# Kernel optimization log

Measured on AMD Instinct MI355X. Metric: run time of the kernel, lower is better.

## Reference

```python
import jax, jax.numpy as jnp
import numpy as np

N_NODES = 40000
N_EDGES = 640000
N_GRAPHS = 64
F_IN = 32       # fourier_order*4
D_EMB = 256     # int(0.5*512)
D_HID = 512     # int(0.5*1024)
D_FC = 1024     # int(0.5*2048)
N_CLS = 10


def setup_inputs() -> dict:
    key = jax.random.key(0)
    ks = iter(jax.random.split(key, 40))
    rn = lambda shape, s=0.05: jax.random.normal(next(ks), shape, jnp.float32) * s
    inp = {
        'x': jax.random.normal(next(ks), (N_NODES, F_IN), jnp.float32),
        'edge_index': jax.random.randint(next(ks), (2, N_EDGES), 0, N_NODES, jnp.int32),
        'edge_attr': jax.random.uniform(next(ks), (N_EDGES, 1), jnp.float32),
        'batch': jnp.sort(jax.random.randint(next(ks), (N_NODES,), 0, N_GRAPHS, jnp.int32)),
        # embedding MLP
        'emb_w1': rn((F_IN, D_EMB)), 'emb_b1': jnp.zeros((D_EMB,), jnp.float32),
        'emb_w2': rn((D_EMB, D_EMB)), 'emb_b2': jnp.zeros((D_EMB,), jnp.float32),
        # edge_proj MLP
        'ep_w1': rn((1, 64)), 'ep_b1': jnp.zeros((64,), jnp.float32),
        'ep_w2': rn((64, 1)), 'ep_b2': jnp.zeros((1,), jnp.float32),
        # GCNConv weights (x @ W + b, PyG convention)
        'w_c1': rn((D_EMB, D_HID)), 'b_c1': jnp.zeros((D_HID,), jnp.float32),
        'w_c2': rn((D_HID, D_HID)), 'b_c2': jnp.zeros((D_HID,), jnp.float32),
        'w_c3': rn((D_HID, D_HID)), 'b_c3': jnp.zeros((D_HID,), jnp.float32),
        'w_c4': rn((D_HID, D_HID)), 'b_c4': jnp.zeros((D_HID,), jnp.float32),
        'w_c5': rn((D_HID, D_HID)), 'b_c5': jnp.zeros((D_HID,), jnp.float32),
        'w_c6': rn((D_HID, D_HID)), 'b_c6': jnp.zeros((D_HID,), jnp.float32),
        # head
        'fc1_w': rn((D_HID, D_FC)), 'fc1_b': jnp.zeros((D_FC,), jnp.float32),
        'head_w': rn((D_FC, N_CLS)), 'head_b': jnp.zeros((N_CLS,), jnp.float32),
    }
    return inp


def _gcn_conv(x, src, dst, norm, W, b):
    # PyG GCNConv: linear transform, then normalized scatter-add aggregation, then bias
    h = x @ W                                   # [N, d_out]
    msg = h[src] * norm[:, None]                # [E+N, d_out] gathered messages
    agg = jax.ops.segment_sum(msg, dst, num_segments=N_NODES)
    return agg + b


def _forward(x, edge_attr, emb_w1, emb_b1, emb_w2, emb_b2, ep_w1, ep_b1, ep_w2, ep_b2,
             w_c1, b_c1, w_c2, b_c2, w_c3, b_c3, w_c4, b_c4, w_c5, b_c5, w_c6, b_c6,
             fc1_w, fc1_b, head_w, head_b, edge_index, batch):
    # edge weights from edge_proj MLP (sigmoid output in (0,1))
    ew = jax.nn.sigmoid(jax.nn.relu(edge_attr @ ep_w1 + ep_b1) @ ep_w2 + ep_b2)[:, 0]  # [E]
    # gcn_norm with self loops (identical for every conv layer -> compute once)
    loops = jnp.arange(N_NODES, dtype=edge_index.dtype)
    src = jnp.concatenate([edge_index[0], loops])
    dst = jnp.concatenate([edge_index[1], loops])
    w = jnp.concatenate([ew, jnp.ones((N_NODES,), ew.dtype)])
    deg = jax.ops.segment_sum(w, dst, num_segments=N_NODES)
    dinv = jnp.where(deg > 0, jax.lax.rsqrt(jnp.maximum(deg, 1e-12)), 0.0)
    norm = dinv[src] * w * dinv[dst]            # [E+N]

    h = jax.nn.relu(jax.nn.relu(x @ emb_w1 + emb_b1) @ emb_w2 + emb_b2)
    h = _gcn_conv(h, src, dst, norm, w_c1, b_c1)
    skip = jax.nn.relu(h)
    h = _gcn_conv(skip, src, dst, norm, w_c2, b_c2)
    h = jax.nn.relu(h)
    h = _gcn_conv(h, src, dst, norm, w_c3, b_c3)
    skip = jax.nn.relu(h) + skip                # has_skip=True
    h = _gcn_conv(skip, src, dst, norm, w_c4, b_c4)  # is_deep=True
    h = jax.nn.relu(h)
    h = _gcn_conv(h, src, dst, norm, w_c5, b_c5)
    h = jax.nn.relu(h)
    h = _gcn_conv(h, src, dst, norm, w_c6, b_c6)
    skip = jax.nn.relu(h) + skip

    # global mean pool over graphs
    sums = jax.ops.segment_sum(skip, batch, num_segments=N_GRAPHS)
    cnts = jax.ops.segment_sum(jnp.ones((N_NODES,), skip.dtype), batch, num_segments=N_GRAPHS)
    pooled = sums / jnp.maximum(cnts, 1.0)[:, None]   # [G, D_HID]

    out = jax.nn.relu(pooled @ fc1_w + fc1_b) @ head_w + head_b   # [G, N_CLS]
    return out


def reference(x, edge_index, edge_attr, batch, emb_w1, emb_b1, emb_w2, emb_b2,
              ep_w1, ep_b1, ep_w2, ep_b2, w_c1, b_c1, w_c2, b_c2, w_c3, b_c3,
              w_c4, b_c4, w_c5, b_c5, w_c6, b_c6, fc1_w, fc1_b, head_w, head_b):
    return _forward(x, edge_attr, emb_w1, emb_b1, emb_w2, emb_b2, ep_w1, ep_b1, ep_w2, ep_b2,
                    w_c1, b_c1, w_c2, b_c2, w_c3, b_c3, w_c4, b_c4, w_c5, b_c5, w_c6, b_c6,
                    fc1_w, fc1_b, head_w, head_b, edge_index, batch)
```

## Files before the change

### kernel.cpp

```cpp
#include <hip/hip_runtime.h>
#include <math.h>

#define N_NODES 40000
#define MP      40192
#define NROWB   157
#define N_EDGES 640000
#define N_GRAPHS 64
#define F_IN 32
#define D_EMB 256
#define D_HID 512
#define D_FC 1024
#define N_CLS 10

typedef _Float16 f16x8 __attribute__((ext_vector_type(8)));
typedef float f32x4  __attribute__((ext_vector_type(4)));
typedef unsigned short u16;

template <int N> struct VecU;
template <> struct VecU<2> { typedef unsigned T __attribute__((ext_vector_type(2))); };
template <> struct VecU<4> { typedef unsigned T __attribute__((ext_vector_type(4))); };

__device__ __forceinline__ float h2f(u16 u) {
    union { u16 s; _Float16 h; } v; v.s = u; return (float)v.h;
}
__device__ __forceinline__ u16 f2h(float f) {
    union { u16 s; _Float16 h; } v; v.h = (_Float16)f; return v.s;
}
__device__ __forceinline__ void async16(void* lds, const void* g) {
    __builtin_amdgcn_global_load_lds((const __attribute__((address_space(1))) void*)g,
                                     (__attribute__((address_space(3))) void*)lds, 16, 0, 0);
}

__device__ __forceinline__ int pk_idx(int r, int q) {
    int rp = r >> 1;
    int g  = (((r & 1) << 2) | q) ^ (rp & 7);
    return rp * 64 + g * 8;
}

__global__ void prep_all(const float* __restrict__ x, u16* __restrict__ xb, u16* __restrict__ G,
                         float* __restrict__ deg, int* __restrict__ cnt, int* __restrict__ cursor,
                         float* __restrict__ sums) {
    int i = blockIdx.x * blockDim.x + threadIdx.x;
    if (i < N_NODES) { deg[i] = 1.0f; cnt[i] = 0; cursor[i] = 0; }
    if (i < MP * F_IN) {
        int row = i >> 5, colk = i & 31;
        float v = (row < N_NODES) ? x[i] : 0.f;
        size_t idx = (size_t)(row >> 8) * 8192 + pk_idx(row & 255, colk >> 3) + (colk & 7);
        xb[idx] = f2h(v);
    }
    if (i < 16 * 3072) {
        int kc = i / 3072, rem = i % 3072;
        G[(size_t)(156 * 16 + kc) * 8192 + 5120 + rem] = 0;
    } else if (i < 16 * 3072 + 8 * 3072) {
        int j = i - 16 * 3072;
        int kc = j / 3072, rem = j % 3072;
        G[(size_t)(156 * 8 + kc) * 8192 + 5120 + rem] = 0;
    }
    if (i < N_GRAPHS * D_HID) sums[i] = 0.f;
}

__global__ void edge_mlp_deg(const float* __restrict__ edge_attr,
                             const float* __restrict__ ep_w1, const float* __restrict__ ep_b1,
                             const float* __restrict__ ep_w2, const float* __restrict__ ep_b2,
                             const int* __restrict__ dst,
                             float* __restrict__ ew, float* __restrict__ deg, int* __restrict__ cnt) {
    __shared__ float w1[64], b1[64], w2[64];
    int t = threadIdx.x;
    if (t < 64) { w1[t] = ep_w1[t]; b1[t] = ep_b1[t]; w2[t] = ep_w2[t]; }
    __syncthreads();
    int e = blockIdx.x * blockDim.x + t;
    if (e >= N_EDGES) return;
    float x = edge_attr[e];
    float s = ep_b2[0];
#pragma unroll
    for (int j = 0; j < 64; ++j) s += fmaxf(x * w1[j] + b1[j], 0.f) * w2[j];
    float sig = 1.f / (1.f + expf(-s));
    ew[e] = sig;
    int d = dst[e];
    atomicAdd(&deg[d], sig);
    atomicAdd(&cnt[d], 1);
}

__global__ void dinv_kernel(const float* __restrict__ deg, float* __restrict__ dinv,
                            float* __restrict__ nloop) {
    int i = blockIdx.x * blockDim.x + threadIdx.x;
    if (i >= N_NODES) return;
    float d = deg[i];
    float r = (d > 0.f) ? rsqrtf(fmaxf(d, 1e-12f)) : 0.f;
    dinv[i] = r;
    nloop[i] = r * r;
}

__global__ void scan_kernel(const int* __restrict__ cnt, int* __restrict__ rowptr) {
    __shared__ int part[1024];
    int t = threadIdx.x;
    const int PER = (N_NODES + 1023) / 1024;
    int base = t * PER;
    int s = 0;
    for (int k = 0; k < PER; ++k) { int i = base + k; if (i < N_NODES) s += cnt[i]; }
    part[t] = s;
    __syncthreads();
    for (int off = 1; off < 1024; off <<= 1) {
        int v = (t >= off) ? part[t - off] : 0;
        __syncthreads();
        part[t] += v;
        __syncthreads();
    }
    int run = (t == 0) ? 0 : part[t - 1];
    for (int k = 0; k < PER; ++k) {
        int i = base + k;
        if (i < N_NODES) { rowptr[i] = run; run += cnt[i]; }
    }
    if (t == 1023) rowptr[N_NODES] = run;
}

__global__ void fill_csr_kernel(const int* __restrict__ src, const int* __restrict__ dst,
                                const float* __restrict__ ew, const float* __restrict__ dinv,
                                const int* __restrict__ rowptr, int* __restrict__ cursor,
                                int2* __restrict__ cv) {
    int e = blockIdx.x * blockDim.x + threadIdx.x;
    if (e >= N_EDGES) return;
    int d = dst[e];
    int s = src[e];
    float n = dinv[s] * ew[e] * dinv[d];
    int p = rowptr[d] + atomicAdd(&cursor[d], 1);
    cv[p] = make_int2(s, __float_as_int(n));
}

struct WPair { const float* s; u16* d; int K; int N; };
struct WP8 { WPair m[8]; };

__global__ void wprep_all(WP8 a) {
    __shared__ u16 th[32][33];
    WPair w = a.m[blockIdx.z];
    int n0 = blockIdx.x * 32;
    int k0 = blockIdx.y * 32;
    if (n0 >= w.N || k0 >= w.K) return;
    int tx = threadIdx.x, ty = threadIdx.y;
#pragma unroll
    for (int r = 0; r < 4; ++r) {
        int k = ty + r * 8;
        th[k][tx] = f2h(w.s[(size_t)(k0 + k) * w.N + n0 + tx]);
    }
    __syncthreads();
#pragma unroll
    for (int r = 0; r < 4; ++r) {
        int n = ty + r * 8;
        int R = n0 + n;
        int kcol = k0 + tx;
        size_t idx = ((size_t)(R >> 7) * (w.K >> 5) + (kcol >> 5)) * 4096
                   + pk_idx(R & 127, (kcol >> 3) & 3) + (kcol & 7);
        w.d[idx] = th[tx][n];
    }
}

__launch_bounds__(512)
__global__ void mfma_gemm(const u16* __restrict__ A,
                          const u16* __restrict__ W,
                          const float* __restrict__ bias,
                          const u16* __restrict__ skip,
                          u16* __restrict__ C, u16* __restrict__ Cpk,
                          int K, int N,
                          const int* __restrict__ batch, float* __restrict__ pool) {
    __shared__ __align__(16) u16 smem[2 * 12288];
    __shared__ int sbatch[128];

    int nColB = N >> 7;
    int b = blockIdx.x;
    int rowI = (b >> 3) / nColB * 8 + (b & 7);
    int colI = (b >> 3) % nColB;
    if (rowI >= NROWB) return;
    int rowBase = rowI * 256;
    int colBase = colI * 128;

    int t = threadIdx.x;
    int lane = t & 63;
    int wave = t >> 6;
    int wr = wave >> 1;
    int wc = wave & 1;

    int quad = lane >> 4;
    int mrow = lane & 15;

    const u16* pA = A + (size_t)rowI * (K >> 5) * 8192 + wave * 1024 + (lane << 3);
    const u16* pW = W + (size_t)colI * (K >> 5) * 4096 + wave * 512 + (lane << 3);

    f32x4 acc[4][4] = {};

    int nIter = K >> 5;
    {
        u16* As = smem; u16* Ws = smem + 8192;
        async16(&As[wave * 1024], pA);
        async16(&As[wave * 1024 + 512], pA + 512);
        async16(&Ws[wave * 512], pW);
    }

    for (int it = 0; it < nIter; ++it) {
        int cur = it & 1;
        __builtin_amdgcn_s_barrier();
        if (it + 1 < nIter) {
            u16* As = smem + (cur ^ 1) * 12288; u16* Ws = As + 8192;
            const u16* sA = pA + (size_t)(it + 1) * 8192;
            const u16* sW = pW + (size_t)(it + 1) * 4096;
            async16(&As[wave * 1024], sA);
            async16(&As[wave * 1024 + 512], sA + 512);
            async16(&Ws[wave * 512], sW);
            asm volatile("s_waitcnt vmcnt(3)" ::: "memory");
        } else {
            asm volatile("s_waitcnt vmcnt(0)" ::: "memory");
        }
        __builtin_amdgcn_sched_barrier(0);
        __builtin_amdgcn_s_barrier();
        __builtin_amdgcn_sched_barrier(0);

        const u16* As = smem + cur * 12288;
        const u16* Ws = As + 8192;
        f16x8 af[4], wf[4];
#pragma unroll
        for (int i = 0; i < 4; ++i) {
            int Ra = wr * 64 + i * 16 + mrow;
            int sa = ((Ra & 1) * 4 + quad) ^ ((Ra >> 1) & 7);
            af[i] = *(const f16x8*)&As[(Ra >> 1) * 64 + sa * 8];
            int Rb = wc * 64 + i * 16 + mrow;
            int sb = ((Rb & 1) * 4 + quad) ^ ((Rb >> 1) & 7);
            wf[i] = *(const f16x8*)&Ws[(Rb >> 1) * 64 + sb * 8];
        }
#pragma unroll
        for (int i = 0; i < 4; ++i)
#pragma unroll
            for (int j = 0; j < 4; ++j)
                acc[i][j] = __builtin_amdgcn_mfma_f32_16x16x32_f16(af[i], wf[j], acc[i][j], 0, 0, 0);
    }
    __syncthreads();

    const int ES = 132;
    u16* eb = smem;
#pragma unroll
    for (int ph = 0; ph < 2; ++ph) {
        if ((wr >> 1) == ph) {
#pragma unroll
            for (int j = 0; j < 4; ++j) {
                int col = colBase + wc * 64 + j * 16 + mrow;
                float bv = bias[col];
#pragma unroll
                for (int i = 0; i < 4; ++i) {
#pragma unroll
                    for (int r = 0; r < 4; ++r) {
                        int lr = (wr & 1) * 64 + i * 16 + quad * 4 + r;
                        size_t row = (size_t)rowBase + ph * 128 + lr;
                        float v = fmaxf(acc[i][j][r] + bv, 0.f);
                        if (skip) v += h2f(skip[row * N + col]);
                        eb[lr * ES + wc * 64 + j * 16 + mrow] = f2h(v);
                    }
                }
            }
        }
        if (pool && t < 128) {
            int row = rowBase + ph * 128 + t;
            sbatch[t] = (row < N_NODES) ? batch[row] : -1;
        }
        __syncthreads();
        if (C) {
#pragma unroll
            for (int k2 = 0; k2 < 4; ++k2) {
                int c = t + k2 * 512;
                int row = c >> 4;
                int ch = c & 15;
                f16x8 v = *(const f16x8*)&eb[row * ES + ch * 8];
                *(f16x8*)&C[(size_t)(rowBase + ph * 128 + row) * N + colBase + ch * 8] = v;
            }
        } else if (Cpk) {
#pragma unroll
            for (int k2 = 0; k2 < 4; ++k2) {
                int c = t + k2 * 512;
                int row = c >> 4;
                int ch = c & 15;
                f16x8 v = *(const f16x8*)&eb[row * ES + ch * 8];
                size_t idx = ((size_t)rowI * (N >> 5) + (colBase >> 5) + (ch >> 2)) * 8192
                           + pk_idx(ph * 128 + row, ch & 3);
                *(f16x8*)&Cpk[idx] = v;
            }
        }
        if (pool) {
            int c = t & 127;
            int rs = (t >> 7) * 32;
            float run = 0.f; int g = -1;
            for (int r = rs; r < rs + 32; ++r) {
                int bg = sbatch[r];
                if (bg != g) {
                    if (g >= 0) atomicAdd(&pool[(size_t)g * D_HID + colBase + c], run);
                    run = 0.f; g = bg;
                }
                if (bg >= 0) run += h2f(eb[r * ES + c]);
            }
            if (g >= 0) atomicAdd(&pool[(size_t)g * D_HID + colBase + c], run);
        }
        __syncthreads();
    }
}

template <int D>
__launch_bounds__(256)
__global__ void gather_f16(const u16* __restrict__ h, const int* __restrict__ rowptr,
                           const int2* __restrict__ cv, const float* __restrict__ nloop,
                           u16* __restrict__ out) {
    constexpr int FPL = D / 64;
    constexpr int UPL = FPL / 2;
    using VU = typename VecU<UPL>::T;
    int node = blockIdx.x * 4 + (threadIdx.x >> 6);
    int lane = threadIdx.x & 63;
    if (node >= N_NODES) return;
    union UU { unsigned u; _Float16 h[2]; };
    float acc[FPL];
    float sl = nloop[node];
    {
        VU own = *(const VU*)(h + (size_t)node * D + lane * FPL);
#pragma unroll
        for (int u = 0; u < UPL; ++u) {
            UU w; w.u = own[u];
            acc[2 * u]     = (float)w.h[0] * sl;
            acc[2 * u + 1] = (float)w.h[1] * sl;
        }
    }
    int beg = rowptr[node], end = rowptr[node + 1];
    if (end > beg) {
        int last = end - 1;
        int2 c[8];
#pragma unroll
        for (int m = 0; m < 8; ++m) c[m] = cv[min(beg + m, last)];
        for (int j = beg; j < end; j += 8) {
            VU tv[8];
#pragma unroll
            for (int m = 0; m < 8; ++m)
                tv[m] = *(const VU*)(h + (size_t)c[m].x * D + lane * FPL);
            int jn = j + 8;
            int2 cn[8];
#pragma unroll
            for (int m = 0; m < 8; ++m) cn[m] = c[m];
            if (jn < end) {
#pragma unroll
                for (int m = 0; m < 8; ++m) cn[m] = cv[min(jn + m, last)];
            }
            __builtin_amdgcn_sched_barrier(0);
#pragma unroll
            for (int m = 0; m < 8; ++m) {
                float v = (j + m < end) ? __int_as_float(c[m].y) : 0.f;
#pragma unroll
                for (int u = 0; u < UPL; ++u) {
                    UU w; w.u = tv[m][u];
                    acc[2 * u]     += (float)w.h[0] * v;
                    acc[2 * u + 1] += (float)w.h[1] * v;
                }
            }
#pragma unroll
            for (int m = 0; m < 8; ++m) c[m] = cn[m];
        }
    }
    VU o;
#pragma unroll
    for (int u = 0; u < UPL; ++u) {
        unsigned lo = f2h(acc[2 * u]);
        unsigned hi = f2h(acc[2 * u + 1]);
        o[u] = lo | (hi << 16);
    }
    size_t blkb = (size_t)(node >> 8) * (D >> 5);
    int rr = node & 255;
    if (D == 512) {
        size_t idx = (blkb + (lane >> 2)) * 8192 + pk_idx(rr, lane & 3);
        *(VU*)(out + idx) = o;
    } else {
        size_t idx = (blkb + (lane >> 3)) * 8192 + pk_idx(rr, (lane >> 1) & 3) + (lane & 1) * 4;
        *(VU*)(out + idx) = o;
    }
}

__launch_bounds__(1024)
__global__ void fc1_head(const float* __restrict__ sums, const int* __restrict__ batch,
                         const float* __restrict__ fc1_w, const float* __restrict__ fc1_b,
                         const float* __restrict__ head_w, const float* __restrict__ head_b,
                         float* __restrict__ out) {
    __shared__ float sv[D_HID];
    __shared__ float hacc[N_CLS];
    __shared__ float invc;
    int g = blockIdx.x;
    int t = threadIdx.x;
    if (t == 0) {
        int lo = 0, hi = N_NODES;
        while (lo < hi) { int m = (lo + hi) >> 1; if (batch[m] < g) lo = m + 1; else hi = m; }
        int lb = lo;
        lo = lb; hi = N_NODES;
        while (lo < hi) { int m = (lo + hi) >> 1; if (batch[m] < g + 1) lo = m + 1; else hi = m; }
        invc = 1.f / fmaxf((float)(lo - lb), 1.f);
    }
    if (t < N_CLS) hacc[t] = 0.f;
    __syncthreads();
    if (t < D_HID) sv[t] = sums[(size_t)g * D_HID + t] * invc;
    __syncthreads();
    int j = t;
    float acc = fc1_b[j];
#pragma unroll 8
    for (int k = 0; k < D_HID; ++k) acc += sv[k] * fc1_w[(size_t)k * D_FC + j];
    float f = fmaxf(acc, 0.f);
    float p[N_CLS];
#pragma unroll
    for (int c = 0; c < N_CLS; ++c) p[c] = f * head_w[j * N_CLS + c];
#pragma unroll
    for (int c = 0; c < N_CLS; ++c) {
        float v = p[c];
        for (int off = 32; off; off >>= 1) v += __shfl_down(v, off, 64);
        if ((t & 63) == 0) atomicAdd(&hacc[c], v);
    }
    __syncthreads();
    if (t < N_CLS) out[g * N_CLS + t] = hacc[t] + head_b[t];
}

extern "C" void kernel_launch(void* const* d_in, const int* in_sizes, int n_in,
                              void* d_out, int out_size, void* d_ws, size_t ws_size,
                              hipStream_t stream) {
    const float* x          = (const float*)d_in[0];
    const int*   edge_index = (const int*)d_in[1];
    const float* edge_attr  = (const float*)d_in[2];
    const int*   batch      = (const int*)d_in[3];
    const float* emb_w1 = (const float*)d_in[4];
    const float* emb_b1 = (const float*)d_in[5];
    const float* emb_w2 = (const float*)d_in[6];
    const float* emb_b2 = (const float*)d_in[7];
    const float* ep_w1  = (const float*)d_in[8];
    const float* ep_b1  = (const float*)d_in[9];
    const float* ep_w2  = (const float*)d_in[10];
    const float* ep_b2  = (const float*)d_in[11];
    const float* w_c[6] = { (const float*)d_in[12], (const float*)d_in[14], (const float*)d_in[16],
                            (const float*)d_in[18], (const float*)d_in[20], (const float*)d_in[22] };
    const float* b_c[6] = { (const float*)d_in[13], (const float*)d_in[15], (const float*)d_in[17],
                            (const float*)d_in[19], (const float*)d_in[21], (const float*)d_in[23] };
    const float* fc1_w  = (const float*)d_in[24];
    const float* fc1_b  = (const float*)d_in[25];
    const float* head_w = (const float*)d_in[26];
    const float* head_b = (const float*)d_in[27];
    float* out = (float*)d_out;

    const int* src = edge_index;
    const int* dst = edge_index + N_EDGES;

    char* p = (char*)d_ws;
    auto alloc = [&](size_t bytes) { char* r = p; p += (bytes + 255) & ~(size_t)255; return r; };
    float* ew    = (float*)alloc(N_EDGES * 4);
    float* deg   = (float*)alloc(N_NODES * 4);
    float* dinv  = (float*)alloc(N_NODES * 4);
    float* nloop = (float*)alloc(N_NODES * 4);
    int* cnt     = (int*)alloc(N_NODES * 4);
    int* cursor  = (int*)alloc(N_NODES * 4);
    int* rowptr  = (int*)alloc((N_NODES + 1) * 4);
    int2* cv     = (int2*)alloc((size_t)N_EDGES * 8);
    u16* xb = (u16*)alloc((size_t)MP * F_IN * 2);
    u16* H1 = (u16*)alloc((size_t)MP * D_EMB * 2);
    u16* H2 = (u16*)alloc((size_t)MP * D_EMB * 2);
    u16* G  = (u16*)alloc((size_t)MP * D_HID * 2);
    u16* S1 = (u16*)alloc((size_t)MP * D_HID * 2);
    u16* S2 = (u16*)alloc((size_t)MP * D_HID * 2);
    u16* Cb = (u16*)alloc((size_t)MP * D_HID * 2);
    u16* we1 = (u16*)alloc((size_t)F_IN * D_EMB * 2);
    u16* we2 = (u16*)alloc((size_t)D_EMB * D_EMB * 2);
    u16* wc[6];
    wc[0] = (u16*)alloc((size_t)D_EMB * D_HID * 2);
    for (int i = 1; i < 6; ++i) wc[i] = (u16*)alloc((size_t)D_HID * D_HID * 2);
    float* sums = (float*)alloc(N_GRAPHS * D_HID * 4);

    const int TB = 256;
    const int EB = (N_EDGES + TB - 1) / TB;
    const int NB = (N_NODES + TB - 1) / TB;

    prep_all<<<(MP * F_IN + TB - 1) / TB, TB, 0, stream>>>(x, xb, G, deg, cnt, cursor, sums);
    edge_mlp_deg<<<EB, TB, 0, stream>>>(edge_attr, ep_w1, ep_b1, ep_w2, ep_b2, dst, ew, deg, cnt);
    dinv_kernel<<<NB, TB, 0, stream>>>(deg, dinv, nloop);
    scan_kernel<<<1, 1024, 0, stream>>>(cnt, rowptr);
    fill_csr_kernel<<<EB, TB, 0, stream>>>(src, dst, ew, dinv, rowptr, cursor, cv);

    WP8 wp;
    wp.m[0] = { emb_w1, we1, F_IN,  D_EMB };
    wp.m[1] = { emb_w2, we2, D_EMB, D_EMB };
    wp.m[2] = { w_c[0], wc[0], D_EMB, D_HID };
    for (int i = 1; i < 6; ++i) wp.m[2 + i] = { w_c[i], wc[i], D_HID, D_HID };
    wprep_all<<<dim3(16, 16, 8), dim3(32, 8), 0, stream>>>(wp);

    const int SLOTS = ((NROWB + 7) / 8) * 8;
    const int GRID2 = SLOTS * (D_EMB / 128);
    const int GRID4 = SLOTS * (D_HID / 128);
    mfma_gemm<<<GRID2, 512, 0, stream>>>(xb, we1, emb_b1, nullptr, nullptr, H1, F_IN, D_EMB, nullptr, nullptr);
    mfma_gemm<<<GRID2, 512, 0, stream>>>(H1, we2, emb_b2, nullptr, H2, nullptr, D_EMB, D_EMB, nullptr, nullptr);

    const int GG = (N_NODES + 3) / 4;
    gather_f16<D_EMB><<<GG, 256, 0, stream>>>(H2, rowptr, cv, nloop, G);
    mfma_gemm<<<GRID4, 512, 0, stream>>>(G, wc[0], b_c[0], nullptr, S1, nullptr, D_EMB, D_HID, nullptr, nullptr);
    gather_f16<D_HID><<<GG, 256, 0, stream>>>(S1, rowptr, cv, nloop, G);
    mfma_gemm<<<GRID4, 512, 0, stream>>>(G, wc[1], b_c[1], nullptr, Cb, nullptr, D_HID, D_HID, nullptr, nullptr);
    gather_f16<D_HID><<<GG, 256, 0, stream>>>(Cb, rowptr, cv, nloop, G);
    mfma_gemm<<<GRID4, 512, 0, stream>>>(G, wc[2], b_c[2], S1, S2, nullptr, D_HID, D_HID, nullptr, nullptr);
    gather_f16<D_HID><<<GG, 256, 0, stream>>>(S2, rowptr, cv, nloop, G);
    mfma_gemm<<<GRID4, 512, 0, stream>>>(G, wc[3], b_c[3], nullptr, Cb, nullptr, D_HID, D_HID, nullptr, nullptr);
    gather_f16<D_HID><<<GG, 256, 0, stream>>>(Cb, rowptr, cv, nloop, G);
    mfma_gemm<<<GRID4, 512, 0, stream>>>(G, wc[4], b_c[4], nullptr, Cb, nullptr, D_HID, D_HID, nullptr, nullptr);
    gather_f16<D_HID><<<GG, 256, 0, stream>>>(Cb, rowptr, cv, nloop, G);
    mfma_gemm<<<GRID4, 512, 0, stream>>>(G, wc[5], b_c[5], S2, nullptr, nullptr, D_HID, D_HID, batch, sums);

    fc1_head<<<N_GRAPHS, 1024, 0, stream>>>(sums, batch, fc1_w, fc1_b, head_w, head_b, out);
}
```

Before: 1.206 ms.

## Restructure GEMM to narrow 32-column tiles with full-K weight slice in LDS

The MFMA GEMM switches from 256x128 tiles, where both A and W are double-buffered through LDS, to 256x32 tiles. The whole K-extent weight slice is preloaded into LDS once, and each wave streams its A fragments straight from global memory into registers with software prefetch. This removes per-iteration barriers and LDS staging of A, and the grid grows fourfold for more parallelism. In exchange, each A row block is re-read from global memory by four times as many blocks and per-block MFMA reuse drops, so the kernel may become bandwidth-bound.

```diff
diff --git a/kernel.cpp b/kernel.cpp
--- a/kernel.cpp
+++ b/kernel.cpp
@@ -162,95 +162,99 @@
                           u16* __restrict__ C, u16* __restrict__ Cpk,
                           int K, int N,
                           const int* __restrict__ batch, float* __restrict__ pool) {
-    __shared__ __align__(16) u16 smem[2 * 12288];
+    __shared__ __align__(16) u16 Wl[16384];
     __shared__ int sbatch[128];
 
-    int nColB = N >> 7;
+    const int nColB = N >> 5;
     int b = blockIdx.x;
     int rowI = (b >> 3) / nColB * 8 + (b & 7);
     int colI = (b >> 3) % nColB;
     if (rowI >= NROWB) return;
     int rowBase = rowI * 256;
-    int colBase = colI * 128;
+    int colBase = colI * 32;
 
     int t = threadIdx.x;
     int lane = t & 63;
     int wave = t >> 6;
-    int wr = wave >> 1;
-    int wc = wave & 1;
-
     int quad = lane >> 4;
     int mrow = lane & 15;
-
-    const u16* pA = A + (size_t)rowI * (K >> 5) * 8192 + wave * 1024 + (lane << 3);
-    const u16* pW = W + (size_t)colI * (K >> 5) * 4096 + wave * 512 + (lane << 3);
-
-    f32x4 acc[4][4] = {};
-
     int nIter = K >> 5;
+
+    int sw = (((mrow & 1) << 2) | quad) ^ ((mrow >> 1) & 7);
+    int laneA = (wave * 16 + (mrow >> 1)) * 64 + sw * 8;
+    int laneW = (mrow >> 1) * 64 + sw * 8;
+
+    const u16* pA = A + (size_t)rowI * nIter * 8192;
+
+    f16x8 aA0 = *(const f16x8*)&pA[laneA];
+    f16x8 aA1 = *(const f16x8*)&pA[laneA + 512];
+    f16x8 aB0, aB1;
+
     {
-        u16* As = smem; u16* Ws = smem + 8192;
-        async16(&As[wave * 1024], pA);
-        async16(&As[wave * 1024 + 512], pA + 512);
-        async16(&Ws[wave * 512], pW);
-    }
-
-    for (int it = 0; it < nIter; ++it) {
-        int cur = it & 1;
-        __builtin_amdgcn_s_barrier();
+        const u16* ws = W + ((size_t)(colI >> 2) * nIter) * 4096 + (colI & 3) * 1024;
+        for (int kc = wave; kc < nIter; kc += 8) {
+            const u16* s = ws + (size_t)kc * 4096;
+            async16(&Wl[kc * 1024],       s + lane * 8);
+            async16(&Wl[kc * 1024 + 512], s + 512 + lane * 8);
+        }
+    }
+    asm volatile("s_waitcnt vmcnt(0)" ::: "memory");
+    __syncthreads();
+
+    f32x4 acc[2][2] = {};
+
+    for (int it = 0; it < nIter; it += 2) {
         if (it + 1 < nIter) {
-            u16* As = smem + (cur ^ 1) * 12288; u16* Ws = As + 8192;
-            const u16* sA = pA + (size_t)(it + 1) * 8192;
-            const u16* sW = pW + (size_t)(it + 1) * 4096;
-            async16(&As[wave * 1024], sA);
-            async16(&As[wave * 1024 + 512], sA + 512);
-            async16(&Ws[wave * 512], sW);
-            asm volatile("s_waitcnt vmcnt(3)" ::: "memory");
-        } else {
-            asm volatile("s_waitcnt vmcnt(0)" ::: "memory");
+            const u16* nA = pA + (size_t)(it + 1) * 8192;
+            aB0 = *(const f16x8*)&nA[laneA];
+            aB1 = *(const f16x8*)&nA[laneA + 512];
         }
         __builtin_amdgcn_sched_barrier(0);
-        __builtin_amdgcn_s_barrier();
-        __builtin_amdgcn_sched_barrier(0);
-
-        const u16* As = smem + cur * 12288;
-        const u16* Ws = As + 8192;
-        f16x8 af[4], wf[4];
-#pragma unroll
-        for (int i = 0; i < 4; ++i) {
-            int Ra = wr * 64 + i * 16 + mrow;
-            int sa = ((Ra & 1) * 4 + quad) ^ ((Ra >> 1) & 7);
-            af[i] = *(const f16x8*)&As[(Ra >> 1) * 64 + sa * 8];
-            int Rb = wc * 64 + i * 16 + mrow;
-            int sb = ((Rb & 1) * 4 + quad) ^ ((Rb >> 1) & 7);
-            wf[i] = *(const f16x8*)&Ws[(Rb >> 1) * 64 + sb * 8];
-        }
-#pragma unroll
-        for (int i = 0; i < 4; ++i)
-#pragma unroll
-            for (int j = 0; j < 4; ++j)
-                acc[i][j] = __builtin_amdgcn_mfma_f32_16x16x32_f16(af[i], wf[j], acc[i][j], 0, 0, 0);
-    }
-    __syncthreads();
-
-    const int ES = 132;
-    u16* eb = smem;
+        {
+            const u16* Wc = &Wl[it * 1024];
+            f16x8 w0 = *(const f16x8*)&Wc[laneW];
+            f16x8 w1 = *(const f16x8*)&Wc[laneW + 512];
+            acc[0][0] = __builtin_amdgcn_mfma_f32_16x16x32_f16(aA0, w0, acc[0][0], 0, 0, 0);
+            acc[0][1] = __builtin_amdgcn_mfma_f32_16x16x32_f16(aA0, w1, acc[0][1], 0, 0, 0);
+            acc[1][0] = __builtin_amdgcn_mfma_f32_16x16x32_f16(aA1, w0, acc[1][0], 0, 0, 0);
+            acc[1][1] = __builtin_amdgcn_mfma_f32_16x16x32_f16(aA1, w1, acc[1][1], 0, 0, 0);
+        }
+        if (it + 1 < nIter) {
+            if (it + 2 < nIter) {
+                const u16* nA = pA + (size_t)(it + 2) * 8192;
+                aA0 = *(const f16x8*)&nA[laneA];
+                aA1 = *(const f16x8*)&nA[laneA + 512];
+            }
+            __builtin_amdgcn_sched_barrier(0);
+            const u16* Wc = &Wl[(it + 1) * 1024];
+            f16x8 w0 = *(const f16x8*)&Wc[laneW];
+            f16x8 w1 = *(const f16x8*)&Wc[laneW + 512];
+            acc[0][0] = __builtin_amdgcn_mfma_f32_16x16x32_f16(aB0, w0, acc[0][0], 0, 0, 0);
+            acc[0][1] = __builtin_amdgcn_mfma_f32_16x16x32_f16(aB0, w1, acc[0][1], 0, 0, 0);
+            acc[1][0] = __builtin_amdgcn_mfma_f32_16x16x32_f16(aB1, w0, acc[1][0], 0, 0, 0);
+            acc[1][1] = __builtin_amdgcn_mfma_f32_16x16x32_f16(aB1, w1, acc[1][1], 0, 0, 0);
+        }
+    }
+    __syncthreads();
+
+    u16* eb = Wl;
+    const int ES = 40;
 #pragma unroll
     for (int ph = 0; ph < 2; ++ph) {
-        if ((wr >> 1) == ph) {
-#pragma unroll
-            for (int j = 0; j < 4; ++j) {
-                int col = colBase + wc * 64 + j * 16 + mrow;
+        if ((wave >> 2) == ph) {
+#pragma unroll
+            for (int j = 0; j < 2; ++j) {
+                int col = colBase + j * 16 + mrow;
                 float bv = bias[col];
 #pragma unroll
-                for (int i = 0; i < 4; ++i) {
+                for (int i = 0; i < 2; ++i) {
 #pragma unroll
                     for (int r = 0; r < 4; ++r) {
-                        int lr = (wr & 1) * 64 + i * 16 + quad * 4 + r;
+                        int lr = (wave & 3) * 32 + i * 16 + quad * 4 + r;
                         size_t row = (size_t)rowBase + ph * 128 + lr;
                         float v = fmaxf(acc[i][j][r] + bv, 0.f);
                         if (skip) v += h2f(skip[row * N + col]);
-                        eb[lr * ES + wc * 64 + j * 16 + mrow] = f2h(v);
+                        eb[lr * ES + j * 16 + mrow] = f2h(v);
                     }
                 }
             }
@@ -261,31 +265,21 @@
         }
         __syncthreads();
         if (C) {
-#pragma unroll
-            for (int k2 = 0; k2 < 4; ++k2) {
-                int c = t + k2 * 512;
-                int row = c >> 4;
-                int ch = c & 15;
-                f16x8 v = *(const f16x8*)&eb[row * ES + ch * 8];
-                *(f16x8*)&C[(size_t)(rowBase + ph * 128 + row) * N + colBase + ch * 8] = v;
-            }
+            int row = t >> 2, ch = t & 3;
+            f16x8 v = *(const f16x8*)&eb[row * ES + ch * 8];
+            *(f16x8*)&C[(size_t)(rowBase + ph * 128 + row) * N + colBase + ch * 8] = v;
         } else if (Cpk) {
-#pragma unroll
-            for (int k2 = 0; k2 < 4; ++k2) {
-                int c = t + k2 * 512;
-                int row = c >> 4;
-                int ch = c & 15;
-                f16x8 v = *(const f16x8*)&eb[row * ES + ch * 8];
-                size_t idx = ((size_t)rowI * (N >> 5) + (colBase >> 5) + (ch >> 2)) * 8192
-                           + pk_idx(ph * 128 + row, ch & 3);
-                *(f16x8*)&Cpk[idx] = v;
-            }
-        }
-        if (pool) {
-            int c = t & 127;
-            int rs = (t >> 7) * 32;
+            int row = t >> 2, ch = t & 3;
+            f16x8 v = *(const f16x8*)&eb[row * ES + ch * 8];
+            size_t idx = ((size_t)rowI * (N >> 5) + (colBase >> 5)) * 8192
+                       + pk_idx(ph * 128 + row, ch);
+            *(f16x8*)&Cpk[idx] = v;
+        }
+        if (pool && t < 256) {
+            int c = t & 31;
+            int rs = (t >> 5) * 16;
             float run = 0.f; int g = -1;
-            for (int r = rs; r < rs + 32; ++r) {
+            for (int r = rs; r < rs + 16; ++r) {
                 int bg = sbatch[r];
                 if (bg != g) {
                     if (g >= 0) atomicAdd(&pool[(size_t)g * D_HID + colBase + c], run);
@@ -484,8 +478,8 @@
     wprep_all<<<dim3(16, 16, 8), dim3(32, 8), 0, stream>>>(wp);
 
     const int SLOTS = ((NROWB + 7) / 8) * 8;
-    const int GRID2 = SLOTS * (D_EMB / 128);
-    const int GRID4 = SLOTS * (D_HID / 128);
+    const int GRID2 = SLOTS * (D_EMB / 32);
+    const int GRID4 = SLOTS * (D_HID / 32);
     mfma_gemm<<<GRID2, 512, 0, stream>>>(xb, we1, emb_b1, nullptr, nullptr, H1, F_IN, D_EMB, nullptr, nullptr);
     mfma_gemm<<<GRID2, 512, 0, stream>>>(H1, we2, emb_b2, nullptr, H2, nullptr, D_EMB, D_EMB, nullptr, nullptr);
 
```

Result: faster. 1.121 ms (-7.0%).
